# Optimization experiments

Hardware: AMD Instinct MI355X
Metric: run time of the kernel (lower is better)

The kernel has to match this reference:

```python
import jax, jax.numpy as jnp
import numpy as np

_EPSILON = 1e-06

def _sparsemax(z):
    # sparsemax along last axis (Martins & Astudillo 2016, sort-based projection)
    m = z.shape[-1]
    z_sorted = jnp.flip(jnp.sort(z, axis=-1), axis=-1)          # descending
    z_cum = jnp.cumsum(z_sorted, axis=-1)
    r = jnp.arange(1, m + 1, dtype=z.dtype)
    support = (1.0 + r * z_sorted) > z_cum                       # [b, m]
    k = jnp.sum(support, axis=-1, keepdims=True)                 # support size, int
    tau = (jnp.take_along_axis(z_cum, k - 1, axis=-1) - 1.0) / k.astype(z.dtype)
    return jnp.maximum(z - tau, 0.0)

def setup_inputs() -> dict:
    key = jax.random.key(0)
    ks = jax.random.split(key, 4)
    b, m, d, out = 2048, 8192, 1024, 1000
    encoder_output = jax.random.normal(ks[0], (b, d), dtype=jnp.float32)
    memory_set = jax.random.normal(ks[1], (m, d), dtype=jnp.float32)
    W1 = jax.random.normal(ks[2], (d, 2 * d), dtype=jnp.float32) * (1.0 / np.sqrt(d))
    b1 = jnp.zeros((2 * d,), dtype=jnp.float32)
    W2 = jax.random.normal(ks[3], (2 * d, out), dtype=jnp.float32) * (1.0 / np.sqrt(2 * d))
    b2 = jnp.zeros((out,), dtype=jnp.float32)
    return {"encoder_output": encoder_output, "memory_set": memory_set,
            "W1": W1, "b1": b1, "W2": W2, "b2": b2}

def reference(encoder_output, memory_set, W1, b1, W2, b2):
    # cosine distance: 1 - x_hat @ y_hat^T  (with eps inside the sqrt, as in torch code)
    x_norm = encoder_output / jnp.sqrt(jnp.sum(encoder_output * encoder_output, axis=1, keepdims=True) + _EPSILON)
    y_norm = memory_set / jnp.sqrt(jnp.sum(memory_set * memory_set, axis=1, keepdims=True) + _EPSILON)
    dist = 1.0 - jnp.matmul(x_norm, y_norm.T)                    # [b, m]
    content_weights = _sparsemax(-dist)                          # [b, m]
    memory_vector = jnp.matmul(content_weights, memory_set)      # [b, d]
    h = jax.nn.relu(jnp.matmul(memory_vector, W1) + b1)          # [b, 2d]
    output = jnp.matmul(h, W2) + b2                              # [b, out]
    return output
```

## Files before the change

### kernel.cpp

```cpp
#include <hip/hip_runtime.h>
#include <hip/hip_bf16.h>


#define TPB 256
#define CAP 1024

typedef __bf16 bf16x8 __attribute__((ext_vector_type(8)));
typedef float  f32x4  __attribute__((ext_vector_type(4)));

typedef const __attribute__((address_space(1))) void* gas_ptr;
typedef __attribute__((address_space(3))) void*       las_ptr;

__device__ __forceinline__ unsigned short f2bf(float f) {
    __hip_bfloat16 h = __float2bfloat16(f);
    union { __hip_bfloat16 h; unsigned short s; } u; u.h = h; return u.s;
}
__device__ __forceinline__ float bf2f(unsigned short s) {
    union { unsigned int b; float f; } u; u.b = (unsigned int)s << 16; return u.f;
}
__device__ __forceinline__ unsigned short f2h(float f) {
    union { _Float16 h; unsigned short s; } u; u.h = (_Float16)f; return u.s;
}
__device__ __forceinline__ float h2f(unsigned short s) {
    union { unsigned short s; _Float16 h; } u; u.s = s; return (float)u.h;
}

__device__ __forceinline__ float block_reduce_sum(float v, float* sred) {
    #pragma unroll
    for (int off = 32; off > 0; off >>= 1) v += __shfl_down(v, off, 64);
    int lane = threadIdx.x & 63, wid = threadIdx.x >> 6;
    if (lane == 0) sred[wid] = v;
    __syncthreads();
    if (threadIdx.x == 0) sred[0] = sred[0] + sred[1] + sred[2] + sred[3];
    __syncthreads();
    float r = sred[0];
    __syncthreads();
    return r;
}

__device__ __forceinline__ void block_reduce_sum2(float& a, float& b, float* sred) {
    #pragma unroll
    for (int off = 32; off > 0; off >>= 1) {
        a += __shfl_down(a, off, 64);
        b += __shfl_down(b, off, 64);
    }
    int lane = threadIdx.x & 63, wid = threadIdx.x >> 6;
    if (lane == 0) { sred[wid] = a; sred[4 + wid] = b; }
    __syncthreads();
    if (threadIdx.x == 0) {
        sred[0] = sred[0] + sred[1] + sred[2] + sred[3];
        sred[4] = sred[4] + sred[5] + sred[6] + sred[7];
    }
    __syncthreads();
    a = sred[0]; b = sred[4];
    __syncthreads();
}

__global__ __launch_bounds__(TPB) void normalize_rows_bf16(const float* __restrict__ X0,
                                                           unsigned short* __restrict__ Y0,
                                                           const float* __restrict__ X1,
                                                           unsigned short* __restrict__ Y1,
                                                           float* __restrict__ norms1,
                                                           int nrow0, int cols) {
    __shared__ float sred[4];
    int r = blockIdx.x, tid = threadIdx.x;
    const float* X; unsigned short* Y; float* nn; int row;
    if (r < nrow0) { X = X0; Y = Y0; nn = nullptr; row = r; }
    else           { X = X1; Y = Y1; nn = norms1; row = r - nrow0; }
    const float4* x4 = (const float4*)(X + (size_t)row * cols);
    ushort4* y4 = (ushort4*)(Y + (size_t)row * cols);
    int n4 = cols >> 2;
    float ss = 0.f;
    for (int i = tid; i < n4; i += TPB) {
        float4 v = x4[i];
        ss += v.x * v.x + v.y * v.y + v.z * v.z + v.w * v.w;
    }
    float tot = block_reduce_sum(ss, sred);
    float nrm = sqrtf(tot + 1e-6f);
    float inv = 1.0f / nrm;
    if (nn && tid == 0) nn[row] = nrm;
    for (int i = tid; i < n4; i += TPB) {
        float4 v = x4[i];
        ushort4 o;
        o.x = f2bf(v.x * inv); o.y = f2bf(v.y * inv);
        o.z = f2bf(v.z * inv); o.w = f2bf(v.w * inv);
        y4[i] = o;
    }
}

__device__ __forceinline__ void tc_body(const float* in, unsigned short* out,
                                        int R, int C, int Cpad, int bx, int by) {
    __shared__ float t[32][33];
    int x = threadIdx.x & 31, y = threadIdx.x >> 5;
    int r0 = by * 32, c0 = bx * 32;
    #pragma unroll
    for (int yy = y; yy < 32; yy += 8) {
        int c = c0 + x;
        t[yy][x] = (c < C) ? in[(size_t)(r0 + yy) * C + c] : 0.f;
    }
    __syncthreads();
    #pragma unroll
    for (int yy = y; yy < 32; yy += 8) {
        int c = c0 + yy;
        if (c < Cpad)
            out[(size_t)c * R + r0 + x] = f2bf(t[x][yy]);
    }
}

__global__ __launch_bounds__(TPB) void transpose_cast2(const float* __restrict__ in1,
                                                       unsigned short* __restrict__ out1,
                                                       int R1, int C1, int Cp1,
                                                       const float* __restrict__ in2,
                                                       unsigned short* __restrict__ out2,
                                                       int R2, int C2, int Cp2,
                                                       int nblk1) {
    int bid = blockIdx.x;
    if (bid < nblk1) {
        int nx = Cp1 / 32;
        tc_body(in1, out1, R1, C1, Cp1, bid % nx, bid / nx);
    } else {
        bid -= nblk1;
        int nx = Cp2 / 32;
        tc_body(in2, out2, R2, C2, Cp2, bid % nx, bid / nx);
    }
}

__device__ __forceinline__ void acc8(float* acc, float w, uint4 v) {
    unsigned int ww[4] = {v.x, v.y, v.z, v.w};
    #pragma unroll
    for (int k = 0; k < 4; ++k) {
        acc[2 * k]     += w * bf2f((unsigned short)(ww[k] & 0xffffu));
        acc[2 * k + 1] += w * bf2f((unsigned short)(ww[k] >> 16));
    }
}

__global__ __launch_bounds__(TPB) void sparsemax_gather(const unsigned short* __restrict__ Zh,
                                                        const float* __restrict__ ynorm,
                                                        const unsigned short* __restrict__ yn,
                                                        unsigned short* __restrict__ mv,
                                                        int m, int d) {
    __shared__ unsigned short szh[8192];
    __shared__ float sred[8];
    __shared__ unsigned short cidx[CAP];
    __shared__ float cval[CAP];
    __shared__ unsigned int lcnt;
    int row = blockIdx.x, tid = threadIdx.x;
    const uint4* zr8 = (const uint4*)(Zh + (size_t)row * m);
    uint4* sz8 = (uint4*)szh;
    int n8 = m >> 3;

    float s = 0.f, q = 0.f;
    for (int i = tid; i < n8; i += TPB) {
        uint4 v = zr8[i];
        sz8[i] = v;
        unsigned int ww[4] = {v.x, v.y, v.z, v.w};
        #pragma unroll
        for (int k = 0; k < 4; ++k) {
            float a = h2f((unsigned short)(ww[k] & 0xffffu));
            float bq = h2f((unsigned short)(ww[k] >> 16));
            s += a + bq; q += a * a + bq * bq;
        }
    }
    if (tid == 0) lcnt = 0;
    block_reduce_sum2(s, q, sred);
    float fm   = (float)m;
    float mean = s / fm;
    float sig  = sqrtf(fmaxf(q / fm - mean * mean, 0.f));
    float tau_s = (s - 1.f) / fm;
    float tau_g = mean + 2.f * sig;

    float Sg = 0.f, cg = 0.f, Ss = 0.f, cs = 0.f;
    for (int i = tid; i < n8; i += TPB) {
        uint4 v = sz8[i];
        unsigned int ww[4] = {v.x, v.y, v.z, v.w};
        #pragma unroll
        for (int k = 0; k < 4; ++k) {
            float a = h2f((unsigned short)(ww[k] & 0xffffu));
            float bq = h2f((unsigned short)(ww[k] >> 16));
            if (a > tau_g) { Sg += a - tau_g; cg += 1.f; }
            if (a > tau_s) { Ss += a - tau_s; cs += 1.f; }
            if (bq > tau_g) { Sg += bq - tau_g; cg += 1.f; }
            if (bq > tau_s) { Ss += bq - tau_s; cs += 1.f; }
        }
    }
    block_reduce_sum2(Sg, cg, sred);
    block_reduce_sum2(Ss, cs, sred);

    float tau_lb, S_act, c_act;
    if (Sg >= 1.f) { tau_lb = tau_g; S_act = Sg + cg * tau_g; c_act = cg; }
    else           { tau_lb = tau_s; S_act = Ss + cs * tau_s; c_act = cs; }
    float tau1 = (S_act - 1.f) / c_act;
    if (tau1 < tau_lb) tau1 = tau_lb;

    for (int i = tid; i < m; i += TPB) {
        float z = h2f(szh[i]);
        if (z > tau1) {
            unsigned int slot = atomicAdd(&lcnt, 1u);
            if (slot < CAP) { cidx[slot] = (unsigned short)i; cval[slot] = z; }
        }
    }
    __syncthreads();

    int fast = (lcnt <= CAP && lcnt > 0);
    float tau = tau1;
    int n = (int)lcnt;
    if (fast) {
        if ((tid >> 6) == 0) {
            int lane = tid & 63;
            float tau_l = tau1, prev = -1.f;
            for (int it = 0; it < 64; ++it) {
                float S = 0.f, c = 0.f;
                for (int jj = lane; jj < n; jj += 64) {
                    float z = cval[jj];
                    if (z > tau_l) { S += z; c += 1.f; }
                }
                #pragma unroll
                for (int off = 32; off > 0; off >>= 1) {
                    S += __shfl_down(S, off, 64);
                    c += __shfl_down(c, off, 64);
                }
                S = __shfl(S, 0, 64);
                c = __shfl(c, 0, 64);
                if (c < 0.5f || c == prev) break;
                tau_l = (S - 1.f) / c; prev = c;
            }
            if (lane == 0) sred[0] = tau_l;
        }
        __syncthreads();
        tau = sred[0];
        for (int jj = tid; jj < n; jj += TPB) {
            float w = cval[jj] - tau;
            cval[jj] = (w > 0.f) ? w * ynorm[cidx[jj]] : 0.f;
        }
        __syncthreads();
    } else {
        float prev = -1.f;
        for (int it = 0; it < 64; ++it) {
            float S = 0.f, c = 0.f;
            for (int i = tid; i < m; i += TPB) {
                float z = h2f(szh[i]);
                if (z > tau) { S += z; c += 1.f; }
            }
            block_reduce_sum2(S, c, sred);
            if (c < 0.5f || c == prev) break;
            tau = (S - 1.f) / c; prev = c;
        }
    }

    int g = tid >> 7;
    int c0 = (tid & 127) * 8;
    float acc[8] = {};
    if (fast) {
        int j = g;
        for (; j + 6 < n; j += 8) {
            int i0 = cidx[j],     i1 = cidx[j + 2];
            int i2 = cidx[j + 4], i3 = cidx[j + 6];
            float w0 = cval[j],     w1 = cval[j + 2];
            float w2 = cval[j + 4], w3 = cval[j + 6];
            uint4 v0 = *(const uint4*)&yn[(size_t)i0 * d + c0];
            uint4 v1 = *(const uint4*)&yn[(size_t)i1 * d + c0];
            uint4 v2 = *(const uint4*)&yn[(size_t)i2 * d + c0];
            uint4 v3 = *(const uint4*)&yn[(size_t)i3 * d + c0];
            acc8(acc, w0, v0); acc8(acc, w1, v1);
            acc8(acc, w2, v2); acc8(acc, w3, v3);
        }
        for (; j < n; j += 2) {
            float w = cval[j];
            int idx = (int)cidx[j];
            uint4 v = *(const uint4*)&yn[(size_t)idx * d + c0];
            acc8(acc, w, v);
        }
    } else {
        for (int i = g; i < m; i += 2) {
            float w = h2f(szh[i]) - tau;
            if (w <= 0.f) continue;
            w *= ynorm[i];
            uint4 v = *(const uint4*)&yn[(size_t)i * d + c0];
            acc8(acc, w, v);
        }
    }
    __syncthreads();
    float* comb = (float*)szh;
    if (g == 1) {
        #pragma unroll
        for (int k = 0; k < 8; ++k) comb[(tid & 127) * 8 + k] = acc[k];
    }
    __syncthreads();
    if (g == 0) {
        #pragma unroll
        for (int k = 0; k < 8; ++k) acc[k] += comb[(tid & 127) * 8 + k];
        unsigned int w0 = f2bf(acc[0]) | ((unsigned int)f2bf(acc[1]) << 16);
        unsigned int w1 = f2bf(acc[2]) | ((unsigned int)f2bf(acc[3]) << 16);
        unsigned int w2 = f2bf(acc[4]) | ((unsigned int)f2bf(acc[5]) << 16);
        unsigned int w3 = f2bf(acc[6]) | ((unsigned int)f2bf(acc[7]) << 16);
        uint4 st = {w0, w1, w2, w3};
        *(uint4*)&mv[(size_t)row * d + c0] = st;
    }
}

template <int BM, int BN, int WM, int WN, int OUTMODE, int RELU, int HASBIAS>
__global__ __launch_bounds__((BM / WM) * (BN / WN) * 64)
void gemm_bt(const unsigned short* __restrict__ A,
             const unsigned short* __restrict__ B,
             const float* __restrict__ bias,
             void* __restrict__ C,
             int M, int K, int lda, int NOUT, int ldc) {
    constexpr int NW   = (BM / WM) * (BN / WN);
    constexpr int TPBL = NW * 64;
    constexpr int ITM  = WM / 16;
    constexpr int ITN  = WN / 16;
    __shared__ unsigned short lA[BM * 64];
    __shared__ unsigned short lB[BN * 64];
    int tid = threadIdx.x;
    int lane = tid & 63, wv = tid >> 6;
    int wm = (wv % (BM / WM)) * WM;
    int wn = (wv / (BM / WM)) * WN;
    int lr = lane & 15, kq = lane >> 4;

    int rowBase = blockIdx.y * BM;
    int colBase = blockIdx.x * BN;

    f32x4 acc[ITM][ITN] = {};

    for (int k0 = 0; k0 < K; k0 += 64) {
        constexpr int AI = BM * 8 / TPBL;
        #pragma unroll
        for (int l = 0; l < AI; ++l) {
            int li = l * TPBL + tid;
            int row = li >> 3, s0 = li & 7;
            int seg = s0 ^ (row & 7);
            const char* gp = (const char*)(A + (size_t)(rowBase + row) * lda + k0) + seg * 16;
            __builtin_amdgcn_global_load_lds((gas_ptr)gp, (las_ptr)((char*)lA + li * 16), 16, 0, 0);
        }
        constexpr int BI = BN * 8 / TPBL;
        #pragma unroll
        for (int l = 0; l < BI; ++l) {
            int li = l * TPBL + tid;
            int row = li >> 3, s0 = li & 7;
            int seg = s0 ^ (row & 7);
            const char* gp = (const char*)(B + (size_t)(colBase + row) * K + k0) + seg * 16;
            __builtin_amdgcn_global_load_lds((gas_ptr)gp, (las_ptr)((char*)lB + li * 16), 16, 0, 0);
        }
        __syncthreads();

        #pragma unroll
        for (int h = 0; h < 2; ++h) {
            bf16x8 av[ITM], bv[ITN];
            #pragma unroll
            for (int i = 0; i < ITM; ++i) {
                int row = wm + i * 16 + lr;
                av[i] = *(const bf16x8*)((const char*)lA + row * 128
                                         + ((((h << 2) | kq) ^ (row & 7)) * 16));
            }
            #pragma unroll
            for (int j = 0; j < ITN; ++j) {
                int row = wn + j * 16 + lr;
                bv[j] = *(const bf16x8*)((const char*)lB + row * 128
                                         + ((((h << 2) | kq) ^ (row & 7)) * 16));
            }
            #pragma unroll
            for (int i = 0; i < ITM; ++i)
                #pragma unroll
                for (int j = 0; j < ITN; ++j)
                    acc[i][j] = __builtin_amdgcn_mfma_f32_16x16x32_bf16(av[i], bv[j], acc[i][j], 0, 0, 0);
        }
        __syncthreads();
    }

    float* Cf = (float*)C;
    unsigned short* Cb = (unsigned short*)C;
    bool fullN = (colBase + BN) <= NOUT;
    #pragma unroll
    for (int j = 0; j < ITN; ++j) {
        int col = colBase + wn + j * 16 + lr;
        float bv_ = (HASBIAS && col < NOUT) ? bias[col] : 0.f;
        #pragma unroll
        for (int i = 0; i < ITM; ++i) {
            #pragma unroll
            for (int r = 0; r < 4; ++r) {
                int row = rowBase + wm + i * 16 + kq * 4 + r;
                float v = acc[i][j][r] + bv_;
                if (RELU) v = fmaxf(v, 0.f);
                if (OUTMODE == 0) {
                    float p = __shfl_xor(v, 1, 64);
                    if (fullN) {
                        if (!(lr & 1)) { float2 st = {v, p}; *(float2*)&Cf[(size_t)row * ldc + col] = st; }
                    } else if (col < NOUT) {
                        Cf[(size_t)row * ldc + col] = v;
                    }
                } else {
                    unsigned int hh = (OUTMODE == 1) ? (unsigned int)f2bf(v) : (unsigned int)f2h(v);
                    unsigned int p1 = (unsigned int)__shfl_xor((int)hh, 1, 64);
                    unsigned int u = (hh & 0xffffu) | (p1 << 16);
                    unsigned int p2 = (unsigned int)__shfl_xor((int)u, 2, 64);
                    if (fullN) {
                        if (!(lr & 3)) { uint2 st = {u, p2}; *(uint2*)&Cb[(size_t)row * ldc + col] = st; }
                    } else if (col < NOUT) {
                        Cb[(size_t)row * ldc + col] = (unsigned short)hh;
                    }
                }
            }
        }
    }
}

extern "C" void kernel_launch(void* const* d_in, const int* in_sizes, int n_in,
                              void* d_out, int out_size, void* d_ws, size_t ws_size,
                              hipStream_t stream) {
    const float* enc = (const float*)d_in[0];
    const float* mem = (const float*)d_in[1];
    const float* W1  = (const float*)d_in[2];
    const float* b1  = (const float*)d_in[3];
    const float* W2  = (const float*)d_in[4];
    const float* b2  = (const float*)d_in[5];

    const int d    = in_sizes[3] / 2;
    const int b    = in_sizes[0] / d;
    const int m    = in_sizes[1] / d;
    const int d2   = in_sizes[3];
    const int outN = in_sizes[5];
    const int outPad = 1024;

    unsigned short* xn    = (unsigned short*)d_ws;
    unsigned short* yn    = xn  + (size_t)b * d;
    float*          ynorm = (float*)(yn + (size_t)m * d);
    unsigned short* W1T   = (unsigned short*)(ynorm + m);
    unsigned short* W2T   = W1T + (size_t)d2 * d;
    unsigned short* Zh    = W2T + (size_t)outPad * d2;
    unsigned short* mv    = Zh + (size_t)b * m;
    unsigned short* h     = mv + (size_t)b * d;

    normalize_rows_bf16<<<b + m, TPB, 0, stream>>>(enc, xn, mem, yn, ynorm, b, d);

    int nblk1 = (d2 / 32) * (d / 32);
    int nblk2 = (outPad / 32) * (d2 / 32);
    transpose_cast2<<<nblk1 + nblk2, TPB, 0, stream>>>(W1, W1T, d, d2, d2,
                                                       W2, W2T, d2, outN, outPad, nblk1);

    gemm_bt<256, 128, 64, 64, 2, 0, 0><<<dim3(m / 128, b / 256), 512, 0, stream>>>(
        xn, yn, nullptr, Zh, b, d, d, m, m);

    sparsemax_gather<<<b, TPB, 0, stream>>>(Zh, ynorm, yn, mv, m, d);

    gemm_bt<128, 128, 64, 64, 1, 1, 1><<<dim3(d2 / 128, b / 128), 256, 0, stream>>>(
        mv, W1T, b1, h, b, d, d, d2, d2);

    gemm_bt<128, 64, 32, 64, 0, 0, 1><<<dim3(outPad / 64, b / 128), 256, 0, stream>>>(
        h, W2T, b2, d_out, b, d2, d2, outN, outN);
}
```

Before: 273.8 us.

## Fuse row sum statistics into similarity GEMM epilogue and single-pass sparsemax candidate collection

Result: slower. 321.8 us (+17.5%).

```diff
diff --git a/kernel.cpp b/kernel.cpp
--- a/kernel.cpp
+++ b/kernel.cpp
@@ -61,9 +61,14 @@
                                                            const float* __restrict__ X1,
                                                            unsigned short* __restrict__ Y1,
                                                            float* __restrict__ norms1,
+                                                           float* __restrict__ stats,
+                                                           int statsN,
                                                            int nrow0, int cols) {
     __shared__ float sred[4];
     int r = blockIdx.x, tid = threadIdx.x;
+    if (r == 0) {
+        for (int i = tid; i < statsN; i += TPB) stats[i] = 0.f;
+    }
     const float* X; unsigned short* Y; float* nn; int row;
     if (r < nrow0) { X = X0; Y = Y0; nn = nullptr; row = r; }
     else           { X = X1; Y = Y1; nn = norms1; row = r - nrow0; }
@@ -134,116 +139,133 @@
     }
 }
 
+__device__ __forceinline__ float list_michelot_wave0(const float* cval, int n,
+                                                     float tau0, int tid, float* stau) {
+    if ((tid >> 6) == 0) {
+        int lane = tid & 63;
+        float tau_l = tau0, prev = -1.f;
+        for (int it = 0; it < 64; ++it) {
+            float S = 0.f, c = 0.f;
+            for (int jj = lane; jj < n; jj += 64) {
+                float z = cval[jj];
+                if (z > tau_l) { S += z; c += 1.f; }
+            }
+            #pragma unroll
+            for (int off = 32; off > 0; off >>= 1) {
+                S += __shfl_down(S, off, 64);
+                c += __shfl_down(c, off, 64);
+            }
+            S = __shfl(S, 0, 64);
+            c = __shfl(c, 0, 64);
+            if (c < 0.5f || c == prev) break;
+            tau_l = (S - 1.f) / c; prev = c;
+        }
+        if (lane == 0) *stau = tau_l;
+    }
+    __syncthreads();
+    return *stau;
+}
+
 __global__ __launch_bounds__(TPB) void sparsemax_gather(const unsigned short* __restrict__ Zh,
+                                                        const float* __restrict__ stats,
                                                         const float* __restrict__ ynorm,
                                                         const unsigned short* __restrict__ yn,
                                                         unsigned short* __restrict__ mv,
                                                         int m, int d) {
-    __shared__ unsigned short szh[8192];
     __shared__ float sred[8];
     __shared__ unsigned short cidx[CAP];
     __shared__ float cval[CAP];
+    __shared__ float comb[1024];
     __shared__ unsigned int lcnt;
+    __shared__ float stau;
     int row = blockIdx.x, tid = threadIdx.x;
-    const uint4* zr8 = (const uint4*)(Zh + (size_t)row * m);
-    uint4* sz8 = (uint4*)szh;
+    const unsigned short* zrow = Zh + (size_t)row * m;
+    const uint4* zr8 = (const uint4*)zrow;
     int n8 = m >> 3;
 
-    float s = 0.f, q = 0.f;
+    float S0 = stats[2 * row], Q0 = stats[2 * row + 1];
+    float fm   = (float)m;
+    float mean = S0 / fm;
+    float sig  = sqrtf(fmaxf(Q0 / fm - mean * mean, 0.f));
+    float tau_s = (S0 - 1.f) / fm;
+    float tau_g = mean + 2.f * sig;
+
+    if (tid == 0) lcnt = 0;
+    __syncthreads();
+
+    float Sg = 0.f, cg = 0.f, Ss = 0.f, cs = 0.f;
     for (int i = tid; i < n8; i += TPB) {
         uint4 v = zr8[i];
-        sz8[i] = v;
         unsigned int ww[4] = {v.x, v.y, v.z, v.w};
+        int base = i * 8;
         #pragma unroll
         for (int k = 0; k < 4; ++k) {
-            float a = h2f((unsigned short)(ww[k] & 0xffffu));
+            float a  = h2f((unsigned short)(ww[k] & 0xffffu));
             float bq = h2f((unsigned short)(ww[k] >> 16));
-            s += a + bq; q += a * a + bq * bq;
-        }
-    }
-    if (tid == 0) lcnt = 0;
-    block_reduce_sum2(s, q, sred);
-    float fm   = (float)m;
-    float mean = s / fm;
-    float sig  = sqrtf(fmaxf(q / fm - mean * mean, 0.f));
-    float tau_s = (s - 1.f) / fm;
-    float tau_g = mean + 2.f * sig;
-
-    float Sg = 0.f, cg = 0.f, Ss = 0.f, cs = 0.f;
-    for (int i = tid; i < n8; i += TPB) {
-        uint4 v = sz8[i];
-        unsigned int ww[4] = {v.x, v.y, v.z, v.w};
-        #pragma unroll
-        for (int k = 0; k < 4; ++k) {
-            float a = h2f((unsigned short)(ww[k] & 0xffffu));
-            float bq = h2f((unsigned short)(ww[k] >> 16));
-            if (a > tau_g) { Sg += a - tau_g; cg += 1.f; }
+            if (a > tau_g) {
+                Sg += a - tau_g; cg += 1.f;
+                unsigned int slot = atomicAdd(&lcnt, 1u);
+                if (slot < CAP) { cidx[slot] = (unsigned short)(base + 2 * k); cval[slot] = a; }
+            }
             if (a > tau_s) { Ss += a - tau_s; cs += 1.f; }
-            if (bq > tau_g) { Sg += bq - tau_g; cg += 1.f; }
+            if (bq > tau_g) {
+                Sg += bq - tau_g; cg += 1.f;
+                unsigned int slot = atomicAdd(&lcnt, 1u);
+                if (slot < CAP) { cidx[slot] = (unsigned short)(base + 2 * k + 1); cval[slot] = bq; }
+            }
             if (bq > tau_s) { Ss += bq - tau_s; cs += 1.f; }
         }
     }
     block_reduce_sum2(Sg, cg, sred);
     block_reduce_sum2(Ss, cs, sred);
 
-    float tau_lb, S_act, c_act;
-    if (Sg >= 1.f) { tau_lb = tau_g; S_act = Sg + cg * tau_g; c_act = cg; }
-    else           { tau_lb = tau_s; S_act = Ss + cs * tau_s; c_act = cs; }
-    float tau1 = (S_act - 1.f) / c_act;
-    if (tau1 < tau_lb) tau1 = tau_lb;
-
-    for (int i = tid; i < m; i += TPB) {
-        float z = h2f(szh[i]);
-        if (z > tau1) {
-            unsigned int slot = atomicAdd(&lcnt, 1u);
-            if (slot < CAP) { cidx[slot] = (unsigned short)i; cval[slot] = z; }
-        }
-    }
-    __syncthreads();
-
-    int fast = (lcnt <= CAP && lcnt > 0);
-    float tau = tau1;
-    int n = (int)lcnt;
-    if (fast) {
-        if ((tid >> 6) == 0) {
-            int lane = tid & 63;
-            float tau_l = tau1, prev = -1.f;
-            for (int it = 0; it < 64; ++it) {
-                float S = 0.f, c = 0.f;
-                for (int jj = lane; jj < n; jj += 64) {
-                    float z = cval[jj];
-                    if (z > tau_l) { S += z; c += 1.f; }
-                }
-                #pragma unroll
-                for (int off = 32; off > 0; off >>= 1) {
-                    S += __shfl_down(S, off, 64);
-                    c += __shfl_down(c, off, 64);
-                }
-                S = __shfl(S, 0, 64);
-                c = __shfl(c, 0, 64);
-                if (c < 0.5f || c == prev) break;
-                tau_l = (S - 1.f) / c; prev = c;
-            }
-            if (lane == 0) sred[0] = tau_l;
-        }
-        __syncthreads();
-        tau = sred[0];
+    int fast = 0, n = 0;
+    float tau = tau_s;
+    if (Sg >= 1.f && lcnt > 0 && lcnt <= CAP) {
+        fast = 1; n = (int)lcnt;
+        float tau1 = (Sg + cg * tau_g - 1.f) / cg;
+        if (tau1 < tau_g) tau1 = tau_g;
+        tau = list_michelot_wave0(cval, n, tau1, tid, &stau);
         for (int jj = tid; jj < n; jj += TPB) {
             float w = cval[jj] - tau;
             cval[jj] = (w > 0.f) ? w * ynorm[cidx[jj]] : 0.f;
         }
         __syncthreads();
     } else {
-        float prev = -1.f;
-        for (int it = 0; it < 64; ++it) {
-            float S = 0.f, c = 0.f;
-            for (int i = tid; i < m; i += TPB) {
-                float z = h2f(szh[i]);
-                if (z > tau) { S += z; c += 1.f; }
-            }
-            block_reduce_sum2(S, c, sred);
-            if (c < 0.5f || c == prev) break;
-            tau = (S - 1.f) / c; prev = c;
+        float tau1s = (Ss + cs * tau_s - 1.f) / cs;
+        if (tau1s < tau_s) tau1s = tau_s;
+        __syncthreads();
+        if (tid == 0) lcnt = 0;
+        __syncthreads();
+        for (int i = tid; i < m; i += TPB) {
+            float z = h2f(zrow[i]);
+            if (z > tau1s) {
+                unsigned int slot = atomicAdd(&lcnt, 1u);
+                if (slot < CAP) { cidx[slot] = (unsigned short)i; cval[slot] = z; }
+            }
+        }
+        __syncthreads();
+        if (lcnt > 0 && lcnt <= CAP) {
+            fast = 1; n = (int)lcnt;
+            tau = list_michelot_wave0(cval, n, tau1s, tid, &stau);
+            for (int jj = tid; jj < n; jj += TPB) {
+                float w = cval[jj] - tau;
+                cval[jj] = (w > 0.f) ? w * ynorm[cidx[jj]] : 0.f;
+            }
+            __syncthreads();
+        } else {
+            tau = tau1s;
+            float prev = -1.f;
+            for (int it = 0; it < 64; ++it) {
+                float S = 0.f, c = 0.f;
+                for (int i = tid; i < m; i += TPB) {
+                    float z = h2f(zrow[i]);
+                    if (z > tau) { S += z; c += 1.f; }
+                }
+                block_reduce_sum2(S, c, sred);
+                if (c < 0.5f || c == prev) break;
+                tau = (S - 1.f) / c; prev = c;
+            }
         }
     }
 
@@ -272,7 +294,7 @@
         }
     } else {
         for (int i = g; i < m; i += 2) {
-            float w = h2f(szh[i]) - tau;
+            float w = h2f(zrow[i]) - tau;
             if (w <= 0.f) continue;
             w *= ynorm[i];
             uint4 v = *(const uint4*)&yn[(size_t)i * d + c0];
@@ -280,7 +302,6 @@
         }
     }
     __syncthreads();
-    float* comb = (float*)szh;
     if (g == 1) {
         #pragma unroll
         for (int k = 0; k < 8; ++k) comb[(tid & 127) * 8 + k] = acc[k];
@@ -298,12 +319,13 @@
     }
 }
 
-template <int BM, int BN, int WM, int WN, int OUTMODE, int RELU, int HASBIAS>
+template <int BM, int BN, int WM, int WN, int OUTMODE, int RELU, int HASBIAS, int STATS>
 __global__ __launch_bounds__((BM / WM) * (BN / WN) * 64)
 void gemm_bt(const unsigned short* __restrict__ A,
              const unsigned short* __restrict__ B,
              const float* __restrict__ bias,
              void* __restrict__ C,
+             float* __restrict__ stats,
              int M, int K, int lda, int NOUT, int ldc) {
     constexpr int NW   = (BM / WM) * (BN / WN);
     constexpr int TPBL = NW * 64;
@@ -365,6 +387,31 @@
                     acc[i][j] = __builtin_amdgcn_mfma_f32_16x16x32_bf16(av[i], bv[j], acc[i][j], 0, 0, 0);
         }
         __syncthreads();
+    }
+
+    if (STATS) {
+        #pragma unroll
+        for (int i = 0; i < ITM; ++i) {
+            #pragma unroll
+            for (int r = 0; r < 4; ++r) {
+                float sp = 0.f, qp = 0.f;
+                #pragma unroll
+                for (int j = 0; j < ITN; ++j) {
+                    float v = acc[i][j][r];
+                    sp += v; qp += v * v;
+                }
+                #pragma unroll
+                for (int off = 1; off <= 8; off <<= 1) {
+                    sp += __shfl_xor(sp, off, 64);
+                    qp += __shfl_xor(qp, off, 64);
+                }
+                if (lr == 0) {
+                    int row = rowBase + wm + i * 16 + kq * 4 + r;
+                    atomicAdd(&stats[2 * row], sp);
+                    atomicAdd(&stats[2 * row + 1], qp);
+                }
+            }
+        }
     }
 
     float* Cf = (float*)C;
@@ -429,22 +476,24 @@
     unsigned short* Zh    = W2T + (size_t)outPad * d2;
     unsigned short* mv    = Zh + (size_t)b * m;
     unsigned short* h     = mv + (size_t)b * d;
-
-    normalize_rows_bf16<<<b + m, TPB, 0, stream>>>(enc, xn, mem, yn, ynorm, b, d);
+    float*          stats = (float*)(h + (size_t)b * d2);
+
+    normalize_rows_bf16<<<b + m, TPB, 0, stream>>>(enc, xn, mem, yn, ynorm,
+                                                   stats, 2 * b, b, d);
 
     int nblk1 = (d2 / 32) * (d / 32);
     int nblk2 = (outPad / 32) * (d2 / 32);
     transpose_cast2<<<nblk1 + nblk2, TPB, 0, stream>>>(W1, W1T, d, d2, d2,
                                                        W2, W2T, d2, outN, outPad, nblk1);
 
-    gemm_bt<256, 128, 64, 64, 2, 0, 0><<<dim3(m / 128, b / 256), 512, 0, stream>>>(
-        xn, yn, nullptr, Zh, b, d, d, m, m);
-
-    sparsemax_gather<<<b, TPB, 0, stream>>>(Zh, ynorm, yn, mv, m, d);
-
-    gemm_bt<128, 128, 64, 64, 1, 1, 1><<<dim3(d2 / 128, b / 128), 256, 0, stream>>>(
-        mv, W1T, b1, h, b, d, d, d2, d2);
-
-    gemm_bt<128, 64, 32, 64, 0, 0, 1><<<dim3(outPad / 64, b / 128), 256, 0, stream>>>(
-        h, W2T, b2, d_out, b, d2, d2, outN, outN);
-}
+    gemm_bt<256, 128, 64, 64, 2, 0, 0, 1><<<dim3(m / 128, b / 256), 512, 0, stream>>>(
+        xn, yn, nullptr, Zh, stats, b, d, d, m, m);
+
+    sparsemax_gather<<<b, TPB, 0, stream>>>(Zh, stats, ynorm, yn, mv, m, d);
+
+    gemm_bt<128, 128, 64, 64, 1, 1, 1, 0><<<dim3(d2 / 128, b / 128), 256, 0, stream>>>(
+        mv, W1T, b1, h, nullptr, b, d, d, d2, d2);
+
+    gemm_bt<128, 64, 32, 64, 0, 0, 1, 0><<<dim3(outPad / 64, b / 128), 256, 0, stream>>>(
+        h, W2T, b2, d_out, nullptr, b, d2, d2, outN, outN);
+}
```
